# Optimization experiments

Measured on AMD Instinct MI355X. Metric: run time of the kernel, lower is better.

The kernel has to match this reference:

```python
import jax, jax.numpy as jnp
import numpy as np


def setup_inputs() -> dict:
    key = jax.random.key(0)
    k0, k1, k2, k3 = jax.random.split(key, 4)
    B, V, C, H, W, N = 2, 4, 32, 512, 640, 200000
    feature_maps = jax.random.normal(k0, (B, V, C, H, W), jnp.float32)
    # Points in front of the cameras: z in [1,4], x,y proportional to z so most
    # projections land inside the image (fx=0.8*W, cx=W/2).
    z = jax.random.uniform(k1, (B, 1, N), minval=1.0, maxval=4.0)
    xy = jax.random.uniform(k2, (B, 2, N), minval=-0.4, maxval=0.4) * z
    pts = jnp.concatenate([xy, z], axis=1)  # [B,3,N]
    fx = 0.8 * W
    K = jnp.array([[fx, 0.0, W / 2.0], [0.0, fx, H / 2.0], [0.0, 0.0, 1.0]], jnp.float32)
    cam_intrinsics = jnp.broadcast_to(K, (B, V, 3, 3))
    R = jnp.broadcast_to(jnp.eye(3, dtype=jnp.float32), (B, V, 3, 3))
    t = 0.05 * jax.random.normal(k3, (B, V, 3, 1), jnp.float32)
    cam_extrinsics = jnp.concatenate([R, t], axis=-1)  # [B,V,3,4]
    return {"feature_maps": feature_maps, "pts": pts,
            "cam_intrinsics": cam_intrinsics, "cam_extrinsics": cam_extrinsics}


def _feature_fetch(feature_maps, pts, cam_intrinsics, cam_extrinsics):
    B, V, C, H, W = feature_maps.shape
    N = pts.shape[2]
    BV = B * V
    fm = feature_maps.reshape(BV, C, H, W)
    K = cam_intrinsics.reshape(BV, 3, 3)
    E = cam_extrinsics.reshape(BV, 3, 4)

    # --- projection (torch.no_grad in original -> stop_gradient) ---
    pe = jnp.broadcast_to(pts[:, None], (B, V, 3, N)).reshape(BV, 3, N)
    tp = jnp.einsum('bij,bjn->bin', E[:, :, :3], pe) + E[:, :, 3:4]  # R*p + t, [BV,3,N]
    tp = tp.transpose(0, 2, 1)  # [BV,N,3]
    x, y, z = tp[..., 0], tp[..., 1], tp[..., 2]
    z_zero = z == 0.0
    z_safe = jnp.where(z_zero, 1.0, z)
    normal_uv = jnp.stack([x / z_safe, y / z_safe, jnp.ones_like(x)], axis=-1)  # [BV,N,3]
    uv = jnp.einsum('bnj,bij->bni', normal_uv, K)[..., :2]  # [BV,N,2]
    u = jnp.where(z_zero, 2.0 * W, uv[..., 0])
    v = jnp.where(z_zero, 2.0 * H, uv[..., 1])
    gx = (u - 0.5) / float(W - 1) * 2.0 - 1.0
    gy = (v - 0.5) / float(H - 1) * 2.0 - 1.0
    gx = jax.lax.stop_gradient(gx)
    gy = jax.lax.stop_gradient(gy)

    # --- bilinear grid_sample, align_corners=True, zeros padding ---
    ix = (gx + 1.0) * 0.5 * (W - 1)  # pixel x, [BV,N]
    iy = (gy + 1.0) * 0.5 * (H - 1)
    x0 = jnp.floor(ix)
    y0 = jnp.floor(iy)
    x1, y1 = x0 + 1.0, y0 + 1.0
    wx1 = ix - x0
    wx0 = 1.0 - wx1
    wy1 = iy - y0
    wy0 = 1.0 - wy1

    fm_flat = fm.reshape(BV, C, H * W)

    def corner(xi, yi, w):
        valid = (xi >= 0) & (xi <= W - 1) & (yi >= 0) & (yi <= H - 1)
        xc = jnp.clip(xi, 0, W - 1).astype(jnp.int32)
        yc = jnp.clip(yi, 0, H - 1).astype(jnp.int32)
        idx = yc * W + xc  # [BV,N]
        vals = jnp.take_along_axis(fm_flat, idx[:, None, :], axis=2)  # [BV,C,N]
        return vals * (w * valid.astype(w.dtype))[:, None, :]

    out = (corner(x0, y0, wx0 * wy0) + corner(x1, y0, wx1 * wy0)
           + corner(x0, y1, wx0 * wy1) + corner(x1, y1, wx1 * wy1))
    return out.reshape(B, V, C, N)


def reference(feature_maps, pts, cam_intrinsics, cam_extrinsics):
    return _feature_fetch(feature_maps, pts, cam_intrinsics, cam_extrinsics)
```

## Files before the change

### kernel.cpp

```cpp
#include <hip/hip_runtime.h>

#define BDIM 256

constexpr int Cc = 32, Hh = 512, Ww = 640, HW = Hh * Ww, NBV = 8;

typedef float  fx4 __attribute__((ext_vector_type(4)));
typedef float  fx2 __attribute__((ext_vector_type(2)));
typedef unsigned int ux4 __attribute__((ext_vector_type(4)));

__device__ __forceinline__ unsigned short f32_to_bf16_rne(float f) {
    unsigned int u = __float_as_uint(f);
    u = (u + 0x7fffu + ((u >> 16) & 1u)) >> 16;
    return (unsigned short)u;
}

__global__ __launch_bounds__(256) void transpose_kernel(
    const float* __restrict__ fm, unsigned short* __restrict__ ws)
{
    __shared__ float lds[32 * 260];
    const int bv  = blockIdx.y;
    const int p0  = blockIdx.x * 256;
    const int tid = threadIdx.x;
    const int m   = tid & 63;
    const int g   = tid >> 6;

    const fx4* src = (const fx4*)(fm + (size_t)bv * Cc * HW);
    #pragma unroll
    for (int it = 0; it < 8; ++it) {
        const int c = it * 4 + g;
        fx4 v = __builtin_nontemporal_load(&src[(size_t)((c * HW + p0) >> 2) + m]);
        *(fx4*)&lds[c * 260 + 4 * m] = v;
    }
    __syncthreads();

    const int q     = tid & 7;
    const int pbase = tid >> 3;
    unsigned short* dst = ws + ((size_t)bv * HW + p0) * Cc;
    #pragma unroll
    for (int it = 0; it < 8; ++it) {
        const int pp = it * 32 + pbase;
        ushort4 o;
        o.x = f32_to_bf16_rne(lds[(4 * q + 0) * 260 + pp]);
        o.y = f32_to_bf16_rne(lds[(4 * q + 1) * 260 + pp]);
        o.z = f32_to_bf16_rne(lds[(4 * q + 2) * 260 + pp]);
        o.w = f32_to_bf16_rne(lds[(4 * q + 3) * 260 + pp]);
        *(ushort4*)&dst[(size_t)pp * Cc + 4 * q] = o;
    }
}

__device__ __forceinline__ void project_point(
    const float* Kp, const float* Ep,
    float px, float py, float pz, int* idx, float* wgt)
{
    const float X = fmaf(Ep[0], px, fmaf(Ep[1], py, fmaf(Ep[2], pz, Ep[3])));
    const float Y = fmaf(Ep[4], px, fmaf(Ep[5], py, fmaf(Ep[6], pz, Ep[7])));
    const float Z = fmaf(Ep[8], px, fmaf(Ep[9], py, fmaf(Ep[10], pz, Ep[11])));
    const bool zzero = (Z == 0.0f);
    const float zs = zzero ? 1.0f : Z;
    const float xn = X / zs;
    const float yn = Y / zs;
    float u = fmaf(Kp[0], xn, fmaf(Kp[1], yn, Kp[2]));
    float v = fmaf(Kp[3], xn, fmaf(Kp[4], yn, Kp[5]));
    if (zzero) { u = 2.0f * Ww; v = 2.0f * Hh; }
    const float ix = u - 0.5f;
    const float iy = v - 0.5f;
    const float x0f = floorf(ix);
    const float y0f = floorf(iy);
    const float wx1 = ix - x0f, wx0 = 1.0f - wx1;
    const float wy1 = iy - y0f, wy0 = 1.0f - wy1;
    const bool vx0 = (x0f >= 0.0f)  && (x0f <= (float)(Ww - 1));
    const bool vx1 = (x0f >= -1.0f) && (x0f <= (float)(Ww - 2));
    const bool vy0 = (y0f >= 0.0f)  && (y0f <= (float)(Hh - 1));
    const bool vy1 = (y0f >= -1.0f) && (y0f <= (float)(Hh - 2));
    const int x0c = (int)fminf(fmaxf(x0f,        0.0f), (float)(Ww - 1));
    const int x1c = (int)fminf(fmaxf(x0f + 1.0f, 0.0f), (float)(Ww - 1));
    const int y0c = (int)fminf(fmaxf(y0f,        0.0f), (float)(Hh - 1));
    const int y1c = (int)fminf(fmaxf(y0f + 1.0f, 0.0f), (float)(Hh - 1));
    wgt[0] = wx0 * wy0 * ((vx0 && vy0) ? 1.0f : 0.0f);
    wgt[1] = wx1 * wy0 * ((vx1 && vy0) ? 1.0f : 0.0f);
    wgt[2] = wx0 * wy1 * ((vx0 && vy1) ? 1.0f : 0.0f);
    wgt[3] = wx1 * wy1 * ((vx1 && vy1) ? 1.0f : 0.0f);
    idx[0] = y0c * Ww + x0c;
    idx[1] = y0c * Ww + x1c;
    idx[2] = y1c * Ww + x0c;
    idx[3] = y1c * Ww + x1c;
}

__global__ __launch_bounds__(BDIM) void gather2_kernel(
    const unsigned short* __restrict__ ws,
    const float* __restrict__ pts,
    const float* __restrict__ Kmat,
    const float* __restrict__ Emat,
    float* __restrict__ out,
    int N)
{
    const int bv  = blockIdx.y;
    const int b   = bv >> 2;
    const int tid = threadIdx.x;
    const int q   = tid & 3;
    const int n0  = (blockIdx.x * (BDIM / 4) + (tid >> 2)) * 2;
    if (n0 >= N) return;

    const float* Kp = Kmat + bv * 9;
    const float* Ep = Emat + bv * 12;

    const fx2 pxv = *(const fx2*)&pts[(size_t)(b * 3 + 0) * N + n0];
    const fx2 pyv = *(const fx2*)&pts[(size_t)(b * 3 + 1) * N + n0];
    const fx2 pzv = *(const fx2*)&pts[(size_t)(b * 3 + 2) * N + n0];

    int   idx[2][4];
    float wgt[2][4];
    project_point(Kp, Ep, pxv[0], pyv[0], pzv[0], idx[0], wgt[0]);
    project_point(Kp, Ep, pxv[1], pyv[1], pzv[1], idx[1], wgt[1]);

    const unsigned short* base = ws + (size_t)bv * HW * Cc + q * 8;

    float acc[2][8];
    #pragma unroll
    for (int t = 0; t < 2; ++t)
        #pragma unroll
        for (int j = 0; j < 8; ++j) acc[t][j] = 0.0f;

    #pragma unroll
    for (int t = 0; t < 2; ++t) {
        #pragma unroll
        for (int k = 0; k < 4; ++k) {
            const ux4 vv = *(const ux4*)(base + (size_t)idx[t][k] * Cc);
            const float w = wgt[t][k];
            #pragma unroll
            for (int j = 0; j < 4; ++j) {
                const unsigned int uu = vv[j];
                acc[t][2*j+0] = fmaf(__uint_as_float(uu << 16),         w, acc[t][2*j+0]);
                acc[t][2*j+1] = fmaf(__uint_as_float(uu & 0xffff0000u), w, acc[t][2*j+1]);
            }
        }
    }

    float* obase = out + (size_t)bv * Cc * N + (size_t)(8 * q) * N + n0;
    #pragma unroll
    for (int j = 0; j < 8; ++j) {
        fx2 o = { acc[0][j], acc[1][j] };
        __builtin_nontemporal_store(o, (fx2*)&obase[(size_t)j * N]);
    }
}

__global__ __launch_bounds__(BDIM) void gather_kernel(
    const unsigned short* __restrict__ ws,
    const float* __restrict__ pts,
    const float* __restrict__ Kmat,
    const float* __restrict__ Emat,
    float* __restrict__ out,
    int N)
{
    const int bv  = blockIdx.y;
    const int b   = bv >> 2;
    const int tid = threadIdx.x;
    const int q   = tid & 3;
    const int n   = blockIdx.x * (BDIM / 4) + (tid >> 2);
    if (n >= N) return;

    const float* Kp = Kmat + bv * 9;
    const float* Ep = Emat + bv * 12;

    int   idx[4];
    float wgt[4];
    project_point(Kp, Ep,
                  pts[(size_t)(b * 3 + 0) * N + n],
                  pts[(size_t)(b * 3 + 1) * N + n],
                  pts[(size_t)(b * 3 + 2) * N + n], idx, wgt);

    const unsigned short* base = ws + (size_t)bv * HW * Cc + q * 8;
    float acc[8];
    #pragma unroll
    for (int j = 0; j < 8; ++j) acc[j] = 0.0f;

    #pragma unroll
    for (int k = 0; k < 4; ++k) {
        const ux4 vv = *(const ux4*)(base + (size_t)idx[k] * Cc);
        const float w = wgt[k];
        #pragma unroll
        for (int j = 0; j < 4; ++j) {
            const unsigned int uu = vv[j];
            acc[2*j+0] = fmaf(__uint_as_float(uu << 16),         w, acc[2*j+0]);
            acc[2*j+1] = fmaf(__uint_as_float(uu & 0xffff0000u), w, acc[2*j+1]);
        }
    }

    float* obase = out + (size_t)bv * Cc * N + (size_t)(8 * q) * N + n;
    #pragma unroll
    for (int j = 0; j < 8; ++j)
        __builtin_nontemporal_store(acc[j], &obase[(size_t)j * N]);
}

__global__ __launch_bounds__(BDIM) void feature_fetch_fallback(
    const float* __restrict__ fm, const float* __restrict__ pts,
    const float* __restrict__ Kmat, const float* __restrict__ Emat,
    float* __restrict__ out, int N)
{
    const int bv = blockIdx.y;
    const int b  = bv >> 2;
    const int n  = blockIdx.x * BDIM + threadIdx.x;
    if (n >= N) return;
    const float* Kp = Kmat + bv * 9;
    const float* Ep = Emat + bv * 12;
    int   idx[4];
    float wgt[4];
    project_point(Kp, Ep,
                  pts[(size_t)(b * 3 + 0) * N + n],
                  pts[(size_t)(b * 3 + 1) * N + n],
                  pts[(size_t)(b * 3 + 2) * N + n], idx, wgt);
    const float* basep = fm + (size_t)bv * Cc * HW;
    float* obase = out + (size_t)bv * Cc * N + n;
    #pragma unroll 4
    for (int c = 0; c < Cc; ++c) {
        const float* p = basep + (size_t)c * HW;
        obase[(size_t)c * N] = p[idx[0]] * wgt[0] + p[idx[1]] * wgt[1]
                             + p[idx[2]] * wgt[2] + p[idx[3]] * wgt[3];
    }
}

extern "C" void kernel_launch(void* const* d_in, const int* in_sizes, int n_in,
                              void* d_out, int out_size, void* d_ws, size_t ws_size,
                              hipStream_t stream) {
    const float* fm  = (const float*)d_in[0];
    const float* pts = (const float*)d_in[1];
    const float* K   = (const float*)d_in[2];
    const float* E   = (const float*)d_in[3];
    float* out = (float*)d_out;
    const int N = in_sizes[1] / 6;

    const size_t need = (size_t)NBV * HW * Cc * sizeof(unsigned short);
    if (ws_size >= need) {
        unsigned short* ws = (unsigned short*)d_ws;
        dim3 tgrid(HW / 256, NBV);
        transpose_kernel<<<tgrid, 256, 0, stream>>>(fm, ws);
        if ((N & 1) == 0) {
            const int pts_per_block = (BDIM / 4) * 2;
            dim3 ggrid((N + pts_per_block - 1) / pts_per_block, NBV);
            gather2_kernel<<<ggrid, BDIM, 0, stream>>>(ws, pts, K, E, out, N);
        } else {
            const int pts_per_block = BDIM / 4;
            dim3 ggrid((N + pts_per_block - 1) / pts_per_block, NBV);
            gather_kernel<<<ggrid, BDIM, 0, stream>>>(ws, pts, K, E, out, N);
        }
    } else {
        dim3 grid((N + BDIM - 1) / BDIM, NBV);
        feature_fetch_fallback<<<grid, BDIM, 0, stream>>>(fm, pts, K, E, out, N);
    }
}
```

Measured before the change: 180.3 us.

## Transpose only feature-map tiles touched by projected points

Adds a marking pass that projects every point and sets a per-32x32-tile bitmap, then transposes to bf16 channel-last only the tiles that are marked. The goal is to skip reading and converting unused regions of the feature maps. In return it adds a memset, an extra projection pass with atomics, and a tile transpose whose LDS layout and strided loads may be less efficient. With the test inputs most projections land inside the image, so most tiles are likely marked anyway.

```diff
diff --git a/kernel.cpp b/kernel.cpp
--- a/kernel.cpp
+++ b/kernel.cpp
@@ -3,10 +3,12 @@
 #define BDIM 256
 
 constexpr int Cc = 32, Hh = 512, Ww = 640, HW = Hh * Ww, NBV = 8;
+constexpr int TS = 32, TXN = Ww / TS, TYN = Hh / TS, NTILE = TXN * TYN;
 
 typedef float  fx4 __attribute__((ext_vector_type(4)));
 typedef float  fx2 __attribute__((ext_vector_type(2)));
 typedef unsigned int ux4 __attribute__((ext_vector_type(4)));
+typedef unsigned int ux2 __attribute__((ext_vector_type(2)));
 
 __device__ __forceinline__ unsigned short f32_to_bf16_rne(float f) {
     unsigned int u = __float_as_uint(f);
@@ -14,43 +16,10 @@
     return (unsigned short)u;
 }
 
-__global__ __launch_bounds__(256) void transpose_kernel(
-    const float* __restrict__ fm, unsigned short* __restrict__ ws)
-{
-    __shared__ float lds[32 * 260];
-    const int bv  = blockIdx.y;
-    const int p0  = blockIdx.x * 256;
-    const int tid = threadIdx.x;
-    const int m   = tid & 63;
-    const int g   = tid >> 6;
-
-    const fx4* src = (const fx4*)(fm + (size_t)bv * Cc * HW);
-    #pragma unroll
-    for (int it = 0; it < 8; ++it) {
-        const int c = it * 4 + g;
-        fx4 v = __builtin_nontemporal_load(&src[(size_t)((c * HW + p0) >> 2) + m]);
-        *(fx4*)&lds[c * 260 + 4 * m] = v;
-    }
-    __syncthreads();
-
-    const int q     = tid & 7;
-    const int pbase = tid >> 3;
-    unsigned short* dst = ws + ((size_t)bv * HW + p0) * Cc;
-    #pragma unroll
-    for (int it = 0; it < 8; ++it) {
-        const int pp = it * 32 + pbase;
-        ushort4 o;
-        o.x = f32_to_bf16_rne(lds[(4 * q + 0) * 260 + pp]);
-        o.y = f32_to_bf16_rne(lds[(4 * q + 1) * 260 + pp]);
-        o.z = f32_to_bf16_rne(lds[(4 * q + 2) * 260 + pp]);
-        o.w = f32_to_bf16_rne(lds[(4 * q + 3) * 260 + pp]);
-        *(ushort4*)&dst[(size_t)pp * Cc + 4 * q] = o;
-    }
-}
-
 __device__ __forceinline__ void project_point(
     const float* Kp, const float* Ep,
-    float px, float py, float pz, int* idx, float* wgt)
+    float px, float py, float pz,
+    int& x0c, int& x1c, int& y0c, int& y1c, float* wgt)
 {
     const float X = fmaf(Ep[0], px, fmaf(Ep[1], py, fmaf(Ep[2], pz, Ep[3])));
     const float Y = fmaf(Ep[4], px, fmaf(Ep[5], py, fmaf(Ep[6], pz, Ep[7])));
@@ -72,18 +41,118 @@
     const bool vx1 = (x0f >= -1.0f) && (x0f <= (float)(Ww - 2));
     const bool vy0 = (y0f >= 0.0f)  && (y0f <= (float)(Hh - 1));
     const bool vy1 = (y0f >= -1.0f) && (y0f <= (float)(Hh - 2));
-    const int x0c = (int)fminf(fmaxf(x0f,        0.0f), (float)(Ww - 1));
-    const int x1c = (int)fminf(fmaxf(x0f + 1.0f, 0.0f), (float)(Ww - 1));
-    const int y0c = (int)fminf(fmaxf(y0f,        0.0f), (float)(Hh - 1));
-    const int y1c = (int)fminf(fmaxf(y0f + 1.0f, 0.0f), (float)(Hh - 1));
+    x0c = (int)fminf(fmaxf(x0f,        0.0f), (float)(Ww - 1));
+    x1c = (int)fminf(fmaxf(x0f + 1.0f, 0.0f), (float)(Ww - 1));
+    y0c = (int)fminf(fmaxf(y0f,        0.0f), (float)(Hh - 1));
+    y1c = (int)fminf(fmaxf(y0f + 1.0f, 0.0f), (float)(Hh - 1));
     wgt[0] = wx0 * wy0 * ((vx0 && vy0) ? 1.0f : 0.0f);
     wgt[1] = wx1 * wy0 * ((vx1 && vy0) ? 1.0f : 0.0f);
     wgt[2] = wx0 * wy1 * ((vx0 && vy1) ? 1.0f : 0.0f);
     wgt[3] = wx1 * wy1 * ((vx1 && vy1) ? 1.0f : 0.0f);
-    idx[0] = y0c * Ww + x0c;
-    idx[1] = y0c * Ww + x1c;
-    idx[2] = y1c * Ww + x0c;
-    idx[3] = y1c * Ww + x1c;
+}
+
+__global__ __launch_bounds__(256) void mark_kernel(
+    const float* __restrict__ pts,
+    const float* __restrict__ Kmat,
+    const float* __restrict__ Emat,
+    unsigned int* __restrict__ bitmap,
+    int N)
+{
+    const int bv = blockIdx.y;
+    const int b  = bv >> 2;
+    const int n  = blockIdx.x * 256 + threadIdx.x;
+    if (n >= N) return;
+    int x0c, x1c, y0c, y1c; float w[4];
+    project_point(Kmat + bv * 9, Emat + bv * 12,
+                  pts[(size_t)(b * 3 + 0) * N + n],
+                  pts[(size_t)(b * 3 + 1) * N + n],
+                  pts[(size_t)(b * 3 + 2) * N + n],
+                  x0c, x1c, y0c, y1c, w);
+    const int tx0 = x0c >> 5, tx1 = x1c >> 5;
+    const int ty0 = y0c >> 5, ty1 = y1c >> 5;
+    unsigned int* bm = bitmap + bv * NTILE;
+    unsigned int* p0 = &bm[ty0 * TXN + tx0];
+    if (*p0 == 0u) atomicOr(p0, 1u);
+    if (tx1 != tx0) { unsigned int* p = &bm[ty0 * TXN + tx1]; if (*p == 0u) atomicOr(p, 1u); }
+    if (ty1 != ty0) {
+        unsigned int* p = &bm[ty1 * TXN + tx0]; if (*p == 0u) atomicOr(p, 1u);
+        if (tx1 != tx0) { unsigned int* p2 = &bm[ty1 * TXN + tx1]; if (*p2 == 0u) atomicOr(p2, 1u); }
+    }
+}
+
+__global__ __launch_bounds__(256) void transpose_tiles_kernel(
+    const float* __restrict__ fm, unsigned short* __restrict__ ws,
+    const unsigned int* __restrict__ bitmap)
+{
+    const int bv = blockIdx.y;
+    const int t  = blockIdx.x;
+    if (!bitmap[bv * NTILE + t]) return;
+
+    const int ty = t / TXN, tx = t - ty * TXN;
+    const int y0 = ty * TS, x0 = tx * TS;
+
+    __shared__ unsigned short lds[TS * TS * 36];
+
+    const int tid = threadIdx.x;
+    const float* src = fm + (size_t)bv * Cc * HW;
+
+    const int x2 = tid & 15, yh = tid >> 4;
+    #pragma unroll
+    for (int c = 0; c < Cc; ++c) {
+        #pragma unroll
+        for (int k = 0; k < 2; ++k) {
+            const int y = yh + 16 * k;
+            fx2 v = __builtin_nontemporal_load(
+                (const fx2*)&src[(size_t)c * HW + (size_t)(y0 + y) * Ww + x0 + 2 * x2]);
+            lds[(y * TS + 2 * x2 + 0) * 36 + c] = f32_to_bf16_rne(v[0]);
+            lds[(y * TS + 2 * x2 + 1) * 36 + c] = f32_to_bf16_rne(v[1]);
+        }
+    }
+    __syncthreads();
+
+    const int c4 = tid & 3, pb = tid >> 2;
+    #pragma unroll
+    for (int it = 0; it < 16; ++it) {
+        const int pp = it * 64 + pb;
+        const int y = pp >> 5, x = pp & 31;
+        const ux2 lo = *(const ux2*)&lds[pp * 36 + 8 * c4];
+        const ux2 hi = *(const ux2*)&lds[pp * 36 + 8 * c4 + 4];
+        ux4 o; o[0] = lo[0]; o[1] = lo[1]; o[2] = hi[0]; o[3] = hi[1];
+        unsigned short* dst = ws + ((size_t)bv * HW + (size_t)(y0 + y) * Ww + x0 + x) * Cc + 8 * c4;
+        *(ux4*)dst = o;
+    }
+}
+
+__global__ __launch_bounds__(256) void transpose_kernel(
+    const float* __restrict__ fm, unsigned short* __restrict__ ws)
+{
+    __shared__ float lds[32 * 260];
+    const int bv  = blockIdx.y;
+    const int p0  = blockIdx.x * 256;
+    const int tid = threadIdx.x;
+    const int m   = tid & 63;
+    const int g   = tid >> 6;
+    const fx4* src = (const fx4*)(fm + (size_t)bv * Cc * HW);
+    #pragma unroll
+    for (int it = 0; it < 8; ++it) {
+        const int c = it * 4 + g;
+        fx4 v = __builtin_nontemporal_load(&src[(size_t)((c * HW + p0) >> 2) + m]);
+        *(fx4*)&lds[c * 260 + 4 * m] = v;
+    }
+    __syncthreads();
+    const int q     = tid & 7;
+    const int pbase = tid >> 3;
+    unsigned short* dst = ws + ((size_t)bv * HW + p0) * Cc;
+    #pragma unroll
+    for (int it = 0; it < 8; ++it) {
+        const int pp = it * 32 + pbase;
+        ushort4 o;
+        o.x = f32_to_bf16_rne(lds[(4 * q + 0) * 260 + pp]);
+        o.y = f32_to_bf16_rne(lds[(4 * q + 1) * 260 + pp]);
+        o.z = f32_to_bf16_rne(lds[(4 * q + 2) * 260 + pp]);
+        o.w = f32_to_bf16_rne(lds[(4 * q + 3) * 260 + pp]);
+        *(ushort4*)&dst[(size_t)pp * Cc + 4 * q] = o;
+    }
 }
 
 __global__ __launch_bounds__(BDIM) void gather2_kernel(
@@ -110,8 +179,15 @@
 
     int   idx[2][4];
     float wgt[2][4];
-    project_point(Kp, Ep, pxv[0], pyv[0], pzv[0], idx[0], wgt[0]);
-    project_point(Kp, Ep, pxv[1], pyv[1], pzv[1], idx[1], wgt[1]);
+    #pragma unroll
+    for (int t = 0; t < 2; ++t) {
+        int x0c, x1c, y0c, y1c;
+        project_point(Kp, Ep, pxv[t], pyv[t], pzv[t], x0c, x1c, y0c, y1c, wgt[t]);
+        idx[t][0] = y0c * Ww + x0c;
+        idx[t][1] = y0c * Ww + x1c;
+        idx[t][2] = y1c * Ww + x0c;
+        idx[t][3] = y1c * Ww + x1c;
+    }
 
     const unsigned short* base = ws + (size_t)bv * HW * Cc + q * 8;
 
@@ -159,15 +235,14 @@
     const int n   = blockIdx.x * (BDIM / 4) + (tid >> 2);
     if (n >= N) return;
 
-    const float* Kp = Kmat + bv * 9;
-    const float* Ep = Emat + bv * 12;
-
-    int   idx[4];
-    float wgt[4];
-    project_point(Kp, Ep,
+    int x0c, x1c, y0c, y1c; float wgt[4];
+    project_point(Kmat + bv * 9, Emat + bv * 12,
                   pts[(size_t)(b * 3 + 0) * N + n],
                   pts[(size_t)(b * 3 + 1) * N + n],
-                  pts[(size_t)(b * 3 + 2) * N + n], idx, wgt);
+                  pts[(size_t)(b * 3 + 2) * N + n],
+                  x0c, x1c, y0c, y1c, wgt);
+    const int idx[4] = { y0c * Ww + x0c, y0c * Ww + x1c,
+                         y1c * Ww + x0c, y1c * Ww + x1c };
 
     const unsigned short* base = ws + (size_t)bv * HW * Cc + q * 8;
     float acc[8];
@@ -201,14 +276,14 @@
     const int b  = bv >> 2;
     const int n  = blockIdx.x * BDIM + threadIdx.x;
     if (n >= N) return;
-    const float* Kp = Kmat + bv * 9;
-    const float* Ep = Emat + bv * 12;
-    int   idx[4];
-    float wgt[4];
-    project_point(Kp, Ep,
+    int x0c, x1c, y0c, y1c; float wgt[4];
+    project_point(Kmat + bv * 9, Emat + bv * 12,
                   pts[(size_t)(b * 3 + 0) * N + n],
                   pts[(size_t)(b * 3 + 1) * N + n],
-                  pts[(size_t)(b * 3 + 2) * N + n], idx, wgt);
+                  pts[(size_t)(b * 3 + 2) * N + n],
+                  x0c, x1c, y0c, y1c, wgt);
+    const int idx[4] = { y0c * Ww + x0c, y0c * Ww + x1c,
+                         y1c * Ww + x0c, y1c * Ww + x1c };
     const float* basep = fm + (size_t)bv * Cc * HW;
     float* obase = out + (size_t)bv * Cc * N + n;
     #pragma unroll 4
@@ -229,18 +304,39 @@
     float* out = (float*)d_out;
     const int N = in_sizes[1] / 6;
 
-    const size_t need = (size_t)NBV * HW * Cc * sizeof(unsigned short);
-    if (ws_size >= need) {
+    const size_t tiles_bytes = (size_t)NBV * HW * Cc * sizeof(unsigned short);
+    const size_t bm_bytes    = (size_t)NBV * NTILE * sizeof(unsigned int);
+
+    if (ws_size >= tiles_bytes + bm_bytes) {
+        unsigned short* ws = (unsigned short*)d_ws;
+        unsigned int* bitmap = (unsigned int*)((char*)d_ws + tiles_bytes);
+
+        hipMemsetAsync(bitmap, 0, bm_bytes, stream);
+        dim3 mgrid((N + 255) / 256, NBV);
+        mark_kernel<<<mgrid, 256, 0, stream>>>(pts, K, E, bitmap, N);
+        dim3 tgrid(NTILE, NBV);
+        transpose_tiles_kernel<<<tgrid, 256, 0, stream>>>(fm, ws, bitmap);
+
+        if ((N & 1) == 0) {
+            const int ppb = (BDIM / 4) * 2;
+            dim3 ggrid((N + ppb - 1) / ppb, NBV);
+            gather2_kernel<<<ggrid, BDIM, 0, stream>>>(ws, pts, K, E, out, N);
+        } else {
+            const int ppb = BDIM / 4;
+            dim3 ggrid((N + ppb - 1) / ppb, NBV);
+            gather_kernel<<<ggrid, BDIM, 0, stream>>>(ws, pts, K, E, out, N);
+        }
+    } else if (ws_size >= tiles_bytes) {
         unsigned short* ws = (unsigned short*)d_ws;
         dim3 tgrid(HW / 256, NBV);
         transpose_kernel<<<tgrid, 256, 0, stream>>>(fm, ws);
         if ((N & 1) == 0) {
-            const int pts_per_block = (BDIM / 4) * 2;
-            dim3 ggrid((N + pts_per_block - 1) / pts_per_block, NBV);
+            const int ppb = (BDIM / 4) * 2;
+            dim3 ggrid((N + ppb - 1) / ppb, NBV);
             gather2_kernel<<<ggrid, BDIM, 0, stream>>>(ws, pts, K, E, out, N);
         } else {
-            const int pts_per_block = BDIM / 4;
-            dim3 ggrid((N + pts_per_block - 1) / pts_per_block, NBV);
+            const int ppb = BDIM / 4;
+            dim3 ggrid((N + ppb - 1) / ppb, NBV);
             gather_kernel<<<ggrid, BDIM, 0, stream>>>(ws, pts, K, E, out, N);
         }
     } else {
```

New measurement: 373.1 us. +106.9%, slower.
